# Performance work log

Hardware: AMD Instinct MI355X
Metric: run time of the kernel (lower is better)

Reference implementation:

```python
import jax, jax.numpy as jnp
import numpy as np

N = 100000      # nodes
E = 1600000     # edges
IN = 128        # in_channels
HID = 64        # hidden_channels
HEADS = 2       # gat_heads
NEG_SLOPE = 0.2 # PyG GATConv default leaky_relu slope


def setup_inputs() -> dict:
    key = jax.random.key(0)
    ks = jax.random.split(key, 8)
    x = jax.random.normal(ks[0], (N, IN), jnp.float32)
    edge_index = jax.random.randint(ks[1], (2, E), 0, N, jnp.int32)
    edge_weight = jax.random.uniform(ks[2], (E,), jnp.float32)
    gcn_w = jax.random.normal(ks[3], (IN, HID), jnp.float32) * (1.0 / np.sqrt(IN))
    gcn_b = jnp.zeros((HID,), jnp.float32)
    gat_w = jax.random.normal(ks[4], (HID, HEADS * HID), jnp.float32) * (1.0 / np.sqrt(HID))
    att_src = jax.random.normal(ks[5], (HEADS, HID), jnp.float32) * 0.1
    att_dst = jax.random.normal(ks[6], (HEADS, HID), jnp.float32) * 0.1
    gat_b = jnp.zeros((HID,), jnp.float32)
    return {"x": x, "edge_index": edge_index, "edge_weight": edge_weight,
            "gcn_w": gcn_w, "gcn_b": gcn_b, "gat_w": gat_w,
            "att_src": att_src, "att_dst": att_dst, "gat_b": gat_b}


def _gcn(x, w, b, src, dst, ew, n):
    # PyG GCNConv: add self-loops (weight 1), symmetric deg^{-1/2} norm.
    loop = jnp.arange(n, dtype=src.dtype)
    s = jnp.concatenate([src, loop])
    d = jnp.concatenate([dst, loop])
    wt = jnp.concatenate([ew, jnp.ones((n,), ew.dtype)])
    deg = jax.ops.segment_sum(wt, d, num_segments=n)              # in-degree (weighted)
    dinv = jnp.where(deg > 0, jax.lax.rsqrt(jnp.maximum(deg, 1e-12)), 0.0)
    norm = dinv[s] * wt * dinv[d]                                  # [E+N]
    h = x @ w                                                      # [N, HID]
    out = jax.ops.segment_sum(norm[:, None] * h[s], d, num_segments=n)
    return out + b


def _gat(x, w, a_src, a_dst, b, src, dst, n):
    # PyG GATConv: additive attention, self-loops, segment softmax over dst.
    h = (x @ w).reshape(n, HEADS, HID)                             # [N,H,C]
    score_s = jnp.einsum('nhc,hc->nh', h, a_src)                   # [N,H]
    score_d = jnp.einsum('nhc,hc->nh', h, a_dst)                   # [N,H]
    loop = jnp.arange(n, dtype=src.dtype)
    s = jnp.concatenate([src, loop])
    d = jnp.concatenate([dst, loop])
    alpha = score_s[s] + score_d[d]                                # [E+N,H]
    alpha = jnp.where(alpha >= 0, alpha, NEG_SLOPE * alpha)        # leaky_relu
    amax = jax.lax.stop_gradient(jax.ops.segment_max(alpha, d, num_segments=n))
    ex = jnp.exp(alpha - amax[d])
    denom = jax.ops.segment_sum(ex, d, num_segments=n)
    coef = ex / jnp.maximum(denom[d], 1e-16)                       # [E+N,H]
    out = jax.ops.segment_sum(coef[:, :, None] * h[s], d, num_segments=n)  # [N,H,C]
    return out.mean(axis=1) + b                                    # concat=False -> mean


def reference(x, edge_index, edge_weight, gcn_w, gcn_b, gat_w, att_src, att_dst, gat_b):
    src, dst = edge_index[0], edge_index[1]
    n = x.shape[0]
    h = jax.nn.relu(_gcn(x, gcn_w, gcn_b, src, dst, edge_weight, n))
    out = jax.nn.relu(_gat(h, gat_w, att_src, att_dst, gat_b, src, dst, n))
    return out
```

## Files before the change

kernel.cpp:

```cpp
#include <hip/hip_runtime.h>
#include <hip/hip_fp16.h>
#include <math.h>

#define N_NODES 100000
#define N_EDGES 1600000
#define IN_CH 128
#define HID 64
#define HEADS 2
#define NEG_SLOPE 0.2f

#define NB_SCAN ((N_NODES + 255) / 256)
#define SHARD_SZ 12500

static __device__ inline ushort f2h(float f) { return __half_as_ushort(__float2half(f)); }
static __device__ inline float h2f(ushort u) { return __half2float(__ushort_as_half(u)); }
static __device__ inline void h8f(uint4 u, float f[8]) {
    f[0] = h2f((ushort)(u.x & 0xffff)); f[1] = h2f((ushort)(u.x >> 16));
    f[2] = h2f((ushort)(u.y & 0xffff)); f[3] = h2f((ushort)(u.y >> 16));
    f[4] = h2f((ushort)(u.z & 0xffff)); f[5] = h2f((ushort)(u.z >> 16));
    f[6] = h2f((ushort)(u.w & 0xffff)); f[7] = h2f((ushort)(u.w >> 16));
}
static __device__ inline uint pack2(float a, float b) {
    return (uint)f2h(a) | ((uint)f2h(b) << 16);
}

__device__ inline float leaky(float a) { return (a >= 0.0f) ? a : NEG_SLOPE * a; }


__global__ void k_count(const int* __restrict__ dst, int* count) {
    int e = blockIdx.x * 256 + threadIdx.x;
    if (e < N_EDGES) atomicAdd(&count[dst[e]], 1);
}

__global__ void k_scan_a(const int* __restrict__ count, int* __restrict__ incl,
                         int* __restrict__ bsum) {
    __shared__ int sh[256];
    int tid = threadIdx.x;
    int g = blockIdx.x * 256 + tid;
    int v = (g < N_NODES) ? count[g] : 0;
    sh[tid] = v;
    __syncthreads();
    for (int off = 1; off < 256; off <<= 1) {
        int t = (tid >= off) ? sh[tid - off] : 0;
        __syncthreads();
        sh[tid] += t;
        __syncthreads();
    }
    if (g < N_NODES) incl[g] = sh[tid];
    if (tid == 255) bsum[blockIdx.x] = sh[255];
}

__global__ void k_scan_b(const int* __restrict__ bsum, int* __restrict__ boff) {
    __shared__ int sh[512];
    int tid = threadIdx.x;
    int v = (tid < NB_SCAN) ? bsum[tid] : 0;
    sh[tid] = v;
    __syncthreads();
    for (int off = 1; off < 512; off <<= 1) {
        int t = (tid >= off) ? sh[tid - off] : 0;
        __syncthreads();
        sh[tid] += t;
        __syncthreads();
    }
    if (tid < NB_SCAN) boff[tid] = sh[tid] - v;
}

__global__ void k_scan_c(const int* __restrict__ count, const int* __restrict__ incl,
                         const int* __restrict__ boff, int* rowptr, int* cursor) {
    int g = blockIdx.x * 256 + threadIdx.x;
    if (g >= N_NODES) return;
    int excl = incl[g] - count[g] + boff[blockIdx.x];
    rowptr[g] = excl;
    cursor[g] = excl;
    if (g == N_NODES - 1) rowptr[N_NODES] = incl[g] + boff[blockIdx.x];
}

__global__ void k_scatter(const int* __restrict__ src, const int* __restrict__ dst,
                          const float* __restrict__ ew,
                          int* cursor, int2* __restrict__ ep) {
    int shard = blockIdx.x & 7;
    int e = (blockIdx.x >> 3) * 256 + threadIdx.x;
    if (e >= N_EDGES) return;
    int d = dst[e];
    if (d / SHARD_SZ != shard) return;
    int pos = atomicAdd(&cursor[d], 1);
    ep[pos] = make_int2(src[e], __float_as_int(ew[e]));
}

__global__ void k_deg_dinv(const int* __restrict__ rowptr, const int2* __restrict__ ep,
                           float* __restrict__ dinv) {
    int n = blockIdx.x * 256 + threadIdx.x;
    if (n >= N_NODES) return;
    int r0 = rowptr[n], r1 = rowptr[n + 1];
    float deg = 1.0f;
    for (int i = r0; i < r1; ++i) deg += __int_as_float(ep[i].y);
    dinv[n] = rsqrtf(deg);
}


__global__ __launch_bounds__(256) void k_gemm1(const float* __restrict__ x,
                                               const float* __restrict__ w,
                                               ushort4* __restrict__ h1h) {
    __shared__ float sxT[64][65];
    __shared__ float sw[128][64];
    int t = threadIdx.x;
    int tx = t & 15, ty = t >> 4;
    int row0 = blockIdx.x * 64;
    for (int i = t; i < 128 * 16; i += 256)
        ((float4*)sw)[i] = ((const float4*)w)[i];
    float acc[4][4] = {};
    for (int c = 0; c < 2; ++c) {
        __syncthreads();
        for (int i = t; i < 64 * 16; i += 256) {
            int r = i >> 4, kq = i & 15;
            int row = row0 + r;
            float4 v = make_float4(0.f, 0.f, 0.f, 0.f);
            if (row < N_NODES) v = ((const float4*)x)[row * 32 + c * 16 + kq];
            int k = kq * 4;
            sxT[k][r] = v.x; sxT[k + 1][r] = v.y; sxT[k + 2][r] = v.z; sxT[k + 3][r] = v.w;
        }
        __syncthreads();
        #pragma unroll 8
        for (int k = 0; k < 64; ++k) {
            float a0 = sxT[k][ty * 4], a1 = sxT[k][ty * 4 + 1];
            float a2 = sxT[k][ty * 4 + 2], a3 = sxT[k][ty * 4 + 3];
            float4 bb = *(const float4*)&sw[c * 64 + k][tx * 4];
            acc[0][0] += a0 * bb.x; acc[0][1] += a0 * bb.y; acc[0][2] += a0 * bb.z; acc[0][3] += a0 * bb.w;
            acc[1][0] += a1 * bb.x; acc[1][1] += a1 * bb.y; acc[1][2] += a1 * bb.z; acc[1][3] += a1 * bb.w;
            acc[2][0] += a2 * bb.x; acc[2][1] += a2 * bb.y; acc[2][2] += a2 * bb.z; acc[2][3] += a2 * bb.w;
            acc[3][0] += a3 * bb.x; acc[3][1] += a3 * bb.y; acc[3][2] += a3 * bb.z; acc[3][3] += a3 * bb.w;
        }
    }
    #pragma unroll
    for (int i = 0; i < 4; ++i) {
        int row = row0 + ty * 4 + i;
        if (row < N_NODES) {
            ushort4 o;
            o.x = f2h(acc[i][0]); o.y = f2h(acc[i][1]); o.z = f2h(acc[i][2]); o.w = f2h(acc[i][3]);
            h1h[row * 16 + tx] = o;
        }
    }
}

__global__ __launch_bounds__(256) void k_gemm2(const uint4* __restrict__ a16,
                                               const float* __restrict__ w,
                                               const float* __restrict__ att_src,
                                               const float* __restrict__ att_dst,
                                               ushort4* __restrict__ h2h,
                                               float* __restrict__ ss, float* __restrict__ sd) {
    __shared__ float sxT[64][65];
    __shared__ float swh[64][64];
    int t = threadIdx.x;
    int tx = t & 15, ty = t >> 4;
    int tile = blockIdx.x >> 1, half = blockIdx.x & 1;
    int row0 = tile * 64;
    for (int i = t; i < 64 * 16; i += 256) {
        int k = i >> 4, cq = i & 15;
        float4 v = ((const float4*)(w + k * 128 + half * 64))[cq];
        ((float4*)&swh[k][cq * 4])[0] = v;
    }
    for (int i = t; i < 64 * 8; i += 256) {
        int r = i >> 3, j = i & 7;
        int row = row0 + r;
        float f[8] = {};
        if (row < N_NODES) { uint4 u = a16[row * 8 + j]; h8f(u, f); }
        int k = j * 8;
        #pragma unroll
        for (int m = 0; m < 8; ++m) sxT[k + m][r] = f[m];
    }
    __syncthreads();
    float acc[4][4] = {};
    #pragma unroll 8
    for (int k = 0; k < 64; ++k) {
        float a0 = sxT[k][ty * 4], a1 = sxT[k][ty * 4 + 1];
        float a2 = sxT[k][ty * 4 + 2], a3 = sxT[k][ty * 4 + 3];
        float4 bb = *(const float4*)&swh[k][tx * 4];
        acc[0][0] += a0 * bb.x; acc[0][1] += a0 * bb.y; acc[0][2] += a0 * bb.z; acc[0][3] += a0 * bb.w;
        acc[1][0] += a1 * bb.x; acc[1][1] += a1 * bb.y; acc[1][2] += a1 * bb.z; acc[1][3] += a1 * bb.w;
        acc[2][0] += a2 * bb.x; acc[2][1] += a2 * bb.y; acc[2][2] += a2 * bb.z; acc[2][3] += a2 * bb.w;
        acc[3][0] += a3 * bb.x; acc[3][1] += a3 * bb.y; acc[3][2] += a3 * bb.z; acc[3][3] += a3 * bb.w;
    }
    float as0 = att_src[half * 64 + tx * 4],     as1 = att_src[half * 64 + tx * 4 + 1];
    float as2 = att_src[half * 64 + tx * 4 + 2], as3 = att_src[half * 64 + tx * 4 + 3];
    float ad0 = att_dst[half * 64 + tx * 4],     ad1 = att_dst[half * 64 + tx * 4 + 1];
    float ad2 = att_dst[half * 64 + tx * 4 + 2], ad3 = att_dst[half * 64 + tx * 4 + 3];
    #pragma unroll
    for (int i = 0; i < 4; ++i) {
        int row = row0 + ty * 4 + i;
        float ps = acc[i][0] * as0 + acc[i][1] * as1 + acc[i][2] * as2 + acc[i][3] * as3;
        float pd = acc[i][0] * ad0 + acc[i][1] * ad1 + acc[i][2] * ad2 + acc[i][3] * ad3;
        #pragma unroll
        for (int off = 1; off < 16; off <<= 1) {
            ps += __shfl_xor(ps, off, 64);
            pd += __shfl_xor(pd, off, 64);
        }
        if (row < N_NODES) {
            if (tx == 0) { ss[row * 2 + half] = ps; sd[row * 2 + half] = pd; }
            ushort4 o;
            o.x = f2h(acc[i][0]); o.y = f2h(acc[i][1]); o.z = f2h(acc[i][2]); o.w = f2h(acc[i][3]);
            h2h[row * 32 + half * 16 + tx] = o;
        }
    }
}


__global__ void k_gcn_csr(const int* __restrict__ rowptr, const int2* __restrict__ ep,
                          const float* __restrict__ dinv,
                          const uint4* __restrict__ h1q, const float* __restrict__ b,
                          uint4* __restrict__ agg1h) {
    int t = threadIdx.x;
    int n = blockIdx.x * 4 + (t >> 6);
    if (n >= N_NODES) return;
    int lane = t & 63, q = lane >> 3, r = lane & 7;
    int r0 = rowptr[n], r1 = rowptr[n + 1];
    float dn = dinv[n];
    float acc[8] = {};
    if (q == 0) {
        float f[8]; h8f(h1q[n * 8 + r], f);
        #pragma unroll
        for (int j = 0; j < 8; ++j) acc[j] = dn * f[j];
    }
    for (int i = r0 + q; i < r1; i += 8) {
        int2 e = ep[i];
        float wl = dinv[e.x] * __int_as_float(e.y);
        float f[8]; h8f(h1q[e.x * 8 + r], f);
        #pragma unroll
        for (int j = 0; j < 8; ++j) acc[j] += wl * f[j];
    }
    #pragma unroll
    for (int off = 8; off < 64; off <<= 1) {
        #pragma unroll
        for (int j = 0; j < 8; ++j) acc[j] += __shfl_xor(acc[j], off, 64);
    }
    if (q == 0) {
        float4 b0 = ((const float4*)b)[2 * r], b1 = ((const float4*)b)[2 * r + 1];
        float v0 = fmaxf(acc[0] * dn + b0.x, 0.f), v1 = fmaxf(acc[1] * dn + b0.y, 0.f);
        float v2 = fmaxf(acc[2] * dn + b0.z, 0.f), v3 = fmaxf(acc[3] * dn + b0.w, 0.f);
        float v4 = fmaxf(acc[4] * dn + b1.x, 0.f), v5 = fmaxf(acc[5] * dn + b1.y, 0.f);
        float v6 = fmaxf(acc[6] * dn + b1.z, 0.f), v7 = fmaxf(acc[7] * dn + b1.w, 0.f);
        uint4 o;
        o.x = pack2(v0, v1); o.y = pack2(v2, v3); o.z = pack2(v4, v5); o.w = pack2(v6, v7);
        agg1h[n * 8 + r] = o;
    }
}

__global__ void k_gat_csr(const int* __restrict__ rowptr, const int2* __restrict__ ep,
                          const float* __restrict__ ss, const float* __restrict__ sd,
                          const uint4* __restrict__ h2q, const float* __restrict__ b,
                          float* __restrict__ out) {
    __shared__ __align__(16) float lds[2][64];
    int n = blockIdx.x;
    int t = threadIdx.x;
    int head = t >> 6, lane = t & 63;
    int q = lane >> 3, r = lane & 7;
    int r0 = rowptr[n], r1 = rowptr[n + 1];
    float sdn = sd[n * 2 + head];
    float den = 0.f;
    float acc[8] = {};
    if (q == 0) {
        float exs = __expf(leaky(ss[n * 2 + head] + sdn));
        den = exs;
        float f[8]; h8f(h2q[n * 16 + head * 8 + r], f);
        #pragma unroll
        for (int j = 0; j < 8; ++j) acc[j] = exs * f[j];
    }
    for (int i = r0 + q; i < r1; i += 8) {
        int s = ep[i].x;
        float ex = __expf(leaky(ss[s * 2 + head] + sdn));
        den += ex;
        float f[8]; h8f(h2q[s * 16 + head * 8 + r], f);
        #pragma unroll
        for (int j = 0; j < 8; ++j) acc[j] += ex * f[j];
    }
    #pragma unroll
    for (int off = 8; off < 64; off <<= 1) {
        #pragma unroll
        for (int j = 0; j < 8; ++j) acc[j] += __shfl_xor(acc[j], off, 64);
        den += __shfl_xor(den, off, 64);
    }
    if (q == 0) {
        float inv = 1.0f / fmaxf(den, 1e-16f);
        *(float4*)&lds[head][r * 8]     = make_float4(acc[0] * inv, acc[1] * inv, acc[2] * inv, acc[3] * inv);
        *(float4*)&lds[head][r * 8 + 4] = make_float4(acc[4] * inv, acc[5] * inv, acc[6] * inv, acc[7] * inv);
    }
    __syncthreads();
    if (t < 64) {
        float v = 0.5f * (lds[0][t] + lds[1][t]) + b[t];
        out[n * 64 + t] = fmaxf(v, 0.0f);
    }
}

extern "C" void kernel_launch(void* const* d_in, const int* in_sizes, int n_in,
                              void* d_out, int out_size, void* d_ws, size_t ws_size,
                              hipStream_t stream) {
    const float* x       = (const float*)d_in[0];
    const int*   eidx    = (const int*)d_in[1];
    const float* ew      = (const float*)d_in[2];
    const float* gcn_w   = (const float*)d_in[3];
    const float* gcn_b   = (const float*)d_in[4];
    const float* gat_w   = (const float*)d_in[5];
    const float* att_src = (const float*)d_in[6];
    const float* att_dst = (const float*)d_in[7];
    const float* gat_b   = (const float*)d_in[8];
    float* out = (float*)d_out;

    const int* src = eidx;
    const int* dst = eidx + N_EDGES;

    char* p = (char*)d_ws;
    ushort* agg1h = (ushort*)p; p += sizeof(ushort) * (size_t)N_NODES * 64;
    ushort* h1h   = (ushort*)p; p += sizeof(ushort) * (size_t)N_NODES * 64;
    ushort* h2h   = (ushort*)p; p += sizeof(ushort) * (size_t)N_NODES * 128;
    int2*  ep     = (int2*)p;   p += sizeof(int2) * (size_t)N_EDGES;
    int*   count  = (int*)p;    p += sizeof(int) * N_NODES;
    float* dinv   = (float*)p;  p += sizeof(float) * N_NODES;
    int*   incl   = (int*)p;    p += sizeof(int) * N_NODES;
    int*   rowptr = (int*)p;    p += sizeof(int) * (N_NODES + 1);
    int*   cursor = (int*)p;    p += sizeof(int) * N_NODES;
    float* ss     = (float*)p;  p += sizeof(float) * N_NODES * 2;
    float* sd     = (float*)p;  p += sizeof(float) * N_NODES * 2;
    int*   bsum   = (int*)p;    p += sizeof(int) * NB_SCAN;
    int*   boff   = (int*)p;    p += sizeof(int) * NB_SCAN;

    const int T = 256;
    const int NBe  = (N_EDGES + T - 1) / T;
    const int NBe8 = 8 * NBe;

    hipMemsetAsync(count, 0, sizeof(int) * N_NODES, stream);
    k_count<<<NBe, T, 0, stream>>>(dst, count);
    k_scan_a<<<NB_SCAN, T, 0, stream>>>(count, incl, bsum);
    k_scan_b<<<1, 512, 0, stream>>>(bsum, boff);
    k_scan_c<<<NB_SCAN, T, 0, stream>>>(count, incl, boff, rowptr, cursor);
    k_scatter<<<NBe8, T, 0, stream>>>(src, dst, ew, cursor, ep);
    k_deg_dinv<<<NB_SCAN, T, 0, stream>>>(rowptr, ep, dinv);

    k_gemm1<<<(N_NODES + 63) / 64, T, 0, stream>>>(x, gcn_w, (ushort4*)h1h);
    k_gcn_csr<<<(N_NODES + 3) / 4, T, 0, stream>>>(rowptr, ep, dinv, (const uint4*)h1h, gcn_b, (uint4*)agg1h);

    k_gemm2<<<((N_NODES + 63) / 64) * 2, T, 0, stream>>>((const uint4*)agg1h, gat_w, att_src, att_dst, (ushort4*)h2h, ss, sd);
    k_gat_csr<<<N_NODES, 128, 0, stream>>>(rowptr, ep, ss, sd, (const uint4*)h2h, gat_b, out);
}
```

Baseline: 457.8 us.

## Process one GAT node per wavefront with both heads in 16-lane groups

Restructures the GAT aggregation kernel so each 64-lane wavefront handles one node: 16 lanes cover both heads' 128 features and 4 lane groups stride over edges, with four nodes per 256-thread block. The head-mean is done by a lane shuffle instead of shared memory and __syncthreads, and the output is written as float4 vectors. This aims to make each row gather a contiguous 256-byte read and to cut block count and sync overhead. The trade-off is fewer edges in flight per node (4 instead of 8 per head).

```diff
diff --git a/kernel.cpp b/kernel.cpp
--- a/kernel.cpp
+++ b/kernel.cpp
@@ -248,45 +248,52 @@
                           const float* __restrict__ ss, const float* __restrict__ sd,
                           const uint4* __restrict__ h2q, const float* __restrict__ b,
                           float* __restrict__ out) {
-    __shared__ __align__(16) float lds[2][64];
-    int n = blockIdx.x;
     int t = threadIdx.x;
-    int head = t >> 6, lane = t & 63;
-    int q = lane >> 3, r = lane & 7;
+    int n = blockIdx.x * 4 + (t >> 6);
+    if (n >= N_NODES) return;
+    int lane = t & 63;
+    int g = lane >> 4;
+    int t16 = lane & 15;
+    int head = t16 >> 3;
+    int r = t16 & 7;
     int r0 = rowptr[n], r1 = rowptr[n + 1];
     float sdn = sd[n * 2 + head];
     float den = 0.f;
     float acc[8] = {};
-    if (q == 0) {
+    if (g == 0) {
         float exs = __expf(leaky(ss[n * 2 + head] + sdn));
         den = exs;
-        float f[8]; h8f(h2q[n * 16 + head * 8 + r], f);
+        float f[8]; h8f(h2q[n * 16 + t16], f);
         #pragma unroll
         for (int j = 0; j < 8; ++j) acc[j] = exs * f[j];
     }
-    for (int i = r0 + q; i < r1; i += 8) {
+    for (int i = r0 + g; i < r1; i += 4) {
         int s = ep[i].x;
         float ex = __expf(leaky(ss[s * 2 + head] + sdn));
         den += ex;
-        float f[8]; h8f(h2q[s * 16 + head * 8 + r], f);
+        float f[8]; h8f(h2q[s * 16 + t16], f);
         #pragma unroll
         for (int j = 0; j < 8; ++j) acc[j] += ex * f[j];
     }
     #pragma unroll
-    for (int off = 8; off < 64; off <<= 1) {
+    for (int off = 16; off < 64; off <<= 1) {
         #pragma unroll
         for (int j = 0; j < 8; ++j) acc[j] += __shfl_xor(acc[j], off, 64);
         den += __shfl_xor(den, off, 64);
     }
-    if (q == 0) {
-        float inv = 1.0f / fmaxf(den, 1e-16f);
-        *(float4*)&lds[head][r * 8]     = make_float4(acc[0] * inv, acc[1] * inv, acc[2] * inv, acc[3] * inv);
-        *(float4*)&lds[head][r * 8 + 4] = make_float4(acc[4] * inv, acc[5] * inv, acc[6] * inv, acc[7] * inv);
-    }
-    __syncthreads();
-    if (t < 64) {
-        float v = 0.5f * (lds[0][t] + lds[1][t]) + b[t];
-        out[n * 64 + t] = fmaxf(v, 0.0f);
+    float inv = 1.0f / fmaxf(den, 1e-16f);
+    #pragma unroll
+    for (int j = 0; j < 8; ++j) acc[j] *= inv;
+    float o[8];
+    #pragma unroll
+    for (int j = 0; j < 8; ++j) o[j] = 0.5f * (acc[j] + __shfl_xor(acc[j], 8, 64));
+    if (g == 0 && head == 0) {
+        float4 b0 = ((const float4*)b)[2 * r], b1 = ((const float4*)b)[2 * r + 1];
+        float4* op = (float4*)(out + n * 64 + r * 8);
+        op[0] = make_float4(fmaxf(o[0] + b0.x, 0.f), fmaxf(o[1] + b0.y, 0.f),
+                            fmaxf(o[2] + b0.z, 0.f), fmaxf(o[3] + b0.w, 0.f));
+        op[1] = make_float4(fmaxf(o[4] + b1.x, 0.f), fmaxf(o[5] + b1.y, 0.f),
+                            fmaxf(o[6] + b1.z, 0.f), fmaxf(o[7] + b1.w, 0.f));
     }
 }
 
@@ -338,5 +345,5 @@
     k_gcn_csr<<<(N_NODES + 3) / 4, T, 0, stream>>>(rowptr, ep, dinv, (const uint4*)h1h, gcn_b, (uint4*)agg1h);
 
     k_gemm2<<<((N_NODES + 63) / 64) * 2, T, 0, stream>>>((const uint4*)agg1h, gat_w, att_src, att_dst, (ushort4*)h2h, ss, sd);
-    k_gat_csr<<<N_NODES, 128, 0, stream>>>(rowptr, ep, ss, sd, (const uint4*)h2h, gat_b, out);
-}
+    k_gat_csr<<<(N_NODES + 3) / 4, T, 0, stream>>>(rowptr, ep, ss, sd, (const uint4*)h2h, gat_b, out);
+}
```

Measured after the change: 444.2 us. 3.0% less time.
